# Performance work log

Hardware: AMD Instinct MI355X
Metric: run time of the kernel (lower is better)

## Reference

```python
import jax, jax.numpy as jnp
import numpy as np

N = 729        # problem variables
B = 8          # batch
K = 32         # mixing rank (hard-coded in MixingFunc)
NB = 40        # number of symmetry-basis matrices
MAX_ITER = 10  # coordinate-descent sweeps


def setup_inputs() -> dict:
    key = jax.random.key(0)
    ks = jax.random.split(key, 7)
    coeff = jax.random.normal(ks[0], (NB,), jnp.float32)
    upper = jax.random.normal(ks[1], (N,), jnp.float32)
    basis = jax.random.normal(ks[2], (NB, N, N), jnp.float32)
    z = jax.random.uniform(ks[3], (B, N), jnp.float32)
    is_input = jax.random.randint(ks[4], (B, N), 0, 2).astype(jnp.int32)
    v_init_raw = jax.random.normal(ks[5], (B, N + 1, K), jnp.float32)
    # random permutation of the N non-truth variables (indices 1..N), as in satnet init
    perm = (jax.random.permutation(ks[6], N) + 1).astype(jnp.int32)
    return dict(coeff=coeff, upper=upper, basis=basis, z=z,
                is_input=is_input, v_init_raw=v_init_raw, perm=perm)


def _build_C(coeff, upper, basis):
    # BasisFunc.forward: C = [[0, upper^T], [upper, sum_b coeff_b * basis_b]]
    center = jnp.einsum('b,bij->ij', coeff, basis)              # (N, N)
    top = jnp.concatenate([jnp.zeros((1,), upper.dtype), upper])[None, :]  # (1, N+1)
    bottom = jnp.concatenate([upper[:, None], center], axis=1)  # (N, N+1)
    return jnp.concatenate([top, bottom], axis=0)               # (N+1, N+1)


def _init_V(v_raw, z_full):
    # SATNet init: v0 = random unit truth direction; each v_i is placed on the
    # cone around v0 at angle pi*z_i using a random orthogonal direction.
    v0 = v_raw[:, 0] / jnp.linalg.norm(v_raw[:, 0], axis=-1, keepdims=True)  # (B, K)
    dot = jnp.einsum('bnk,bk->bn', v_raw, v0)
    u = v_raw - dot[..., None] * v0[:, None, :]
    u = u / jnp.maximum(jnp.linalg.norm(u, axis=-1, keepdims=True), 1e-8)
    c = jnp.cos(jnp.pi * z_full)[..., None]
    s = jnp.sin(jnp.pi * z_full)[..., None]
    V = -c * v0[:, None, :] + s * u                              # (B, N+1, K)
    V = V.at[:, 0].set(v0)                                       # truth vector pinned
    return V


def _mix(C, V, is_input_full, perm):
    # SATNet mixing coordinate descent: for each free variable i,
    #   g_i = sum_j C[j,i] v_j - C[i,i] v_i ;  v_i <- -g_i / ||g_i||
    Cdiag = jnp.diagonal(C)
    free = (is_input_full == 0)                                  # (B, N+1)

    def coord_step(V, i):
        g = jnp.einsum('j,bjk->bk', C[:, i], V) - Cdiag[i] * V[:, i]  # (B, K)
        gn = jnp.linalg.norm(g, axis=-1, keepdims=True)
        vnew = -g / jnp.maximum(gn, 1e-8)
        V = V.at[:, i].set(jnp.where(free[:, i][:, None], vnew, V[:, i]))
        return V, None

    def sweep(V, _):
        V, _ = jax.lax.scan(coord_step, V, perm)
        return V, None

    V, _ = jax.lax.scan(jax.checkpoint(sweep), V, None, length=MAX_ITER)
    return V


def reference(coeff, upper, basis, z, is_input, v_init_raw, perm):
    Bn = z.shape[0]
    C = _build_C(coeff, upper, basis)
    z_full = jnp.concatenate([jnp.ones((Bn, 1), z.dtype), z], axis=1)
    ii_full = jnp.concatenate(
        [jnp.ones((Bn, 1), is_input.dtype), is_input], axis=1)
    V = _init_V(v_init_raw, z_full)
    V = _mix(C, V, ii_full, perm)
    v0 = V[:, 0]
    cosang = jnp.clip(-jnp.einsum('bnk,bk->bn', V, v0), -1.0 + 1e-6, 1.0 - 1e-6)
    zo = jnp.arccos(cosang) / jnp.pi
    z_out = jnp.where(ii_full == 1, z_full, zo)
    return z_out[:, 1:]
```

## Files before the change

kernel.cpp:

```cpp
#include <hip/hip_runtime.h>

#define NN   729
#define NF   730
#define BV   8
#define KK   32
#define NBAS 40
#define MAXIT 10
#define PI_F 3.14159265358979323846f

#define MTH   512
#define BT    16
#define AST   448

typedef float v2f __attribute__((ext_vector_type(2)));

__device__ __forceinline__ void fma4(float4& w, float c, const float4& d) {
    w.x = fmaf(c, d.x, w.x); w.y = fmaf(c, d.y, w.y);
    w.z = fmaf(c, d.z, w.z); w.w = fmaf(c, d.w, w.w);
}

__global__ void build_C_kernel(const float* __restrict__ coeff,
                               const float* __restrict__ upper,
                               const float* __restrict__ basis,
                               float* __restrict__ Ct) {
    int idx = blockIdx.x * blockDim.x + threadIdx.x;
    if (idx >= NF * NF) return;
    int i = idx / NF, j = idx - i * NF;
    float val;
    if (i == 0) {
        val = (j == 0) ? 0.f : upper[j - 1];
    } else if (j == 0) {
        val = upper[i - 1];
    } else {
        float acc = 0.f;
        const float* bp = basis + (size_t)(i - 1) * NN + (j - 1);
        #pragma unroll 8
        for (int b = 0; b < NBAS; ++b)
            acc = fmaf(coeff[b], bp[(size_t)b * NN * NN], acc);
        val = acc;
    }
    Ct[(size_t)j * NF + i] = val;
}

__global__ void init_V_kernel(const float* __restrict__ z,
                              const float* __restrict__ vraw,
                              float* __restrict__ V) {
    int g = threadIdx.x >> 5;
    int k = threadIdx.x & 31;
    int row = blockIdx.x * 8 + g;
    int b = row / NF, n = row - b * NF;
    const float* vr = vraw + (size_t)b * NF * KK;

    float v0 = vr[k];
    float s2 = v0 * v0;
    #pragma unroll
    for (int off = 16; off; off >>= 1) s2 += __shfl_xor(s2, off, 32);
    v0 = v0 / sqrtf(s2);

    float vn = vr[(size_t)n * KK + k];
    float d = vn * v0;
    #pragma unroll
    for (int off = 16; off; off >>= 1) d += __shfl_xor(d, off, 32);
    float u = vn - d * v0;
    float un2 = u * u;
    #pragma unroll
    for (int off = 16; off; off >>= 1) un2 += __shfl_xor(un2, off, 32);
    u = u / fmaxf(sqrtf(un2), 1e-8f);

    float zf = (n == 0) ? 1.f : z[b * NN + (n - 1)];
    float c = cosf(PI_F * zf), s = sinf(PI_F * zf);
    float outv = -c * v0 + s * u;
    if (n == 0) outv = v0;
    V[((size_t)b * NF + n) * KK + k] = outv;
}

__global__ void build_act_kernel(const int* __restrict__ is_input,
                                 const int* __restrict__ perm,
                                 int* __restrict__ act, int* __restrict__ nA_arr) {
    int b = blockIdx.x, l = threadIdx.x;
    int base = 0;
    for (int c = 0; c < (NN + 63) / 64; ++c) {
        int idx = c * 64 + l;
        bool f = false; int pi = 0;
        if (idx < NN) { pi = perm[idx]; f = (is_input[b * NN + pi - 1] == 0); }
        unsigned long long m = __ballot(f);
        int pos = __popcll(m & ((1ull << l) - 1ull));
        if (f && base + pos < AST) act[b * AST + base + pos] = pi;
        base += __popcll(m);
    }
    if (base > AST) base = AST;
    if (l == 0) nA_arr[b] = base;
    for (int p = base + l; p < AST; p += 64) act[b * AST + p] = 0;
}

__global__ void gather_CactT_kernel(const float* __restrict__ Ct,
                                    const int* __restrict__ act,
                                    float* __restrict__ CactT) {
    int a = blockIdx.x, b = blockIdx.y;
    __shared__ int acts[AST];
    for (int i = threadIdx.x; i < AST; i += blockDim.x) acts[i] = act[b * AST + i];
    __syncthreads();
    const float* src = Ct + (size_t)acts[a] * NF;
    float* dst = CactT + ((size_t)b * AST + a) * AST;
    for (int t = threadIdx.x; t < AST; t += blockDim.x)
        dst[t] = src[acts[t]];
}

__global__ void init_W_kernel(const float* __restrict__ Ct,
                              const int* __restrict__ act,
                              const int* __restrict__ nA_arr,
                              const float* __restrict__ V,
                              float* __restrict__ Wc,
                              float* __restrict__ Vact) {
    int b = blockIdx.y;
    int a = blockIdx.x * 8 + (threadIdx.x >> 5);
    int k = threadIdx.x & 31;
    int nA = nA_arr[b];
    float w = 0.f;
    int ra = act[b * AST + a];
    float vv = V[((size_t)b * NF + ra) * KK + k];
    if (a < nA) {
        const float* ctr = Ct + (size_t)ra * NF;
        const float* vb = V + (size_t)b * NF * KK + k;
        float acc = 0.f;
        for (int j = 0; j < NF; ++j)
            acc = fmaf(ctr[j], vb[(size_t)j * KK], acc);
        w = acc - ctr[ra] * vv;
    }
    Wc[((size_t)b * AST + a) * KK + k] = w;
    Vact[((size_t)b * AST + a) * KK + k] = vv;
}

__device__ __forceinline__ float rowsum16(float x) {
    int y;
    y = __builtin_amdgcn_update_dpp(0, __float_as_int(x), 0x121, 0xF, 0xF, false);
    x += __int_as_float(y);
    y = __builtin_amdgcn_update_dpp(0, __float_as_int(x), 0x122, 0xF, 0xF, false);
    x += __int_as_float(y);
    y = __builtin_amdgcn_update_dpp(0, __float_as_int(x), 0x124, 0xF, 0xF, false);
    x += __int_as_float(y);
    y = __builtin_amdgcn_update_dpp(0, __float_as_int(x), 0x128, 0xF, 0xF, false);
    x += __int_as_float(y);
    return x;
}

__global__ __launch_bounds__(MTH, 2)
void mix_kernel(const float* __restrict__ CactT_g,
                const float* __restrict__ Wc_g,
                const float* __restrict__ Vact_g,
                const int* __restrict__ act_g,
                const int* __restrict__ nA_arr,
                const int* __restrict__ is_input,
                const float* __restrict__ z,
                const float* __restrict__ Vg,
                float* __restrict__ out) {
    __shared__ __align__(16) float V_c[AST * KK];
    __shared__ __align__(16) float dv_s[2][BT * KK];
    __shared__ __align__(16) float gpub[BT * KK];
    __shared__ __align__(16) float cblk_s[2][BT * BT];
    __shared__ float Cd_s[AST];
    __shared__ int   slot_s[NF];
    __shared__ float ldspad[3200];

    int b = blockIdx.x, tid = threadIdx.x;
    const float* CT = CactT_g + (size_t)b * AST * AST;
    const float* Vact = Vact_g + (size_t)b * AST * KK;
    int nA = nA_arr[b];
    int nblkp = (nA + BT - 1) / BT;
    if (nblkp < 2) nblkp = 2;
    int nAp = nblkp * BT;
    int totB = MAXIT * nblkp;

    int wid = tid >> 6;
    int l64 = tid & 63;
    int lane = tid - 64;
    int kq = lane & 7;
    int rslot = lane >> 3;
    int kp = tid & 15;

    for (int idx = tid; idx < AST * 8; idx += MTH)
        ((float4*)V_c)[idx] = ((const float4*)Vact)[idx];
    if (tid < AST) Cd_s[tid] = CT[(size_t)tid * AST + tid];
    if (tid < nA) slot_s[act_g[b * AST + tid]] = tid;
    if (tid < 256) {
        int t = tid >> 4, u = tid & 15;
        cblk_s[0][t * BT + u] = CT[(size_t)u * AST + t];
    }
    if (tid == 0) ldspad[3199] = 0.f;
    float4 w[8];
    #pragma unroll
    for (int p = 0; p < 8; ++p) {
        float4 zz = {0.f, 0.f, 0.f, 0.f};
        w[p] = zz;
        if (wid >= 1)
            w[p] = *(const float4*)&Wc_g[((size_t)b * AST + rslot + 56 * p) * KK + 4 * kq];
    }
    __syncthreads();

    for (int bi = 0; bi < totB; ++bi) {
        int blk = bi % nblkp, s0 = blk * BT;
        int pblk = (bi - 1 + nblkp) % nblkp, sp0 = pblk * BT;
        int cb = bi & 1, pv = cb ^ 1;
        int sn0 = ((bi + 1) % nblkp) * BT;

        if (wid >= 1) {
            #pragma unroll
            for (int p = 0; p < 8; ++p) {
                int a = rslot + 56 * p;
                if ((a >> 4) == blk) {
                    int u = a - s0;
                    if (bi > 0) {
                        const float* cr = CT + (size_t)a * AST + sp0;
                        float4 c0 = *(const float4*)(cr);
                        float4 c1 = *(const float4*)(cr + 4);
                        float4 c2 = *(const float4*)(cr + 8);
                        float4 c3 = *(const float4*)(cr + 12);
                        float4 d;
                        d = *(const float4*)&dv_s[pv][0  * KK + 4 * kq]; fma4(w[p], c0.x, d);
                        d = *(const float4*)&dv_s[pv][1  * KK + 4 * kq]; fma4(w[p], c0.y, d);
                        d = *(const float4*)&dv_s[pv][2  * KK + 4 * kq]; fma4(w[p], c0.z, d);
                        d = *(const float4*)&dv_s[pv][3  * KK + 4 * kq]; fma4(w[p], c0.w, d);
                        d = *(const float4*)&dv_s[pv][4  * KK + 4 * kq]; fma4(w[p], c1.x, d);
                        d = *(const float4*)&dv_s[pv][5  * KK + 4 * kq]; fma4(w[p], c1.y, d);
                        d = *(const float4*)&dv_s[pv][6  * KK + 4 * kq]; fma4(w[p], c1.z, d);
                        d = *(const float4*)&dv_s[pv][7  * KK + 4 * kq]; fma4(w[p], c1.w, d);
                        d = *(const float4*)&dv_s[pv][8  * KK + 4 * kq]; fma4(w[p], c2.x, d);
                        d = *(const float4*)&dv_s[pv][9  * KK + 4 * kq]; fma4(w[p], c2.y, d);
                        d = *(const float4*)&dv_s[pv][10 * KK + 4 * kq]; fma4(w[p], c2.z, d);
                        d = *(const float4*)&dv_s[pv][11 * KK + 4 * kq]; fma4(w[p], c2.w, d);
                        d = *(const float4*)&dv_s[pv][12 * KK + 4 * kq]; fma4(w[p], c3.x, d);
                        d = *(const float4*)&dv_s[pv][13 * KK + 4 * kq]; fma4(w[p], c3.y, d);
                        d = *(const float4*)&dv_s[pv][14 * KK + 4 * kq]; fma4(w[p], c3.z, d);
                        d = *(const float4*)&dv_s[pv][15 * KK + 4 * kq]; fma4(w[p], c3.w, d);
                    }
                    *(float4*)&gpub[u * KK + 4 * kq] = w[p];
                }
            }
        }
        __syncthreads();

        if (wid == 0) {
            float g0[BT], g1[BT], vo0[BT], vo1[BT];
            #pragma unroll
            for (int u = 0; u < BT; ++u) {
                v2f gv = *(const v2f*)&gpub[u * KK + 2 * kp];
                g0[u] = gv.x; g1[u] = gv.y;
                v2f vv = *(const v2f*)&V_c[(s0 + u) * KK + 2 * kp];
                vo0[u] = vv.x; vo1[u] = vv.y;
            }
            #pragma unroll
            for (int u = 0; u < BT; ++u) {
                int s = s0 + u;
                float n2 = fmaf(g0[u], g0[u], g1[u] * g1[u]);
                n2 = rowsum16(n2);
                float inv = -__builtin_amdgcn_rsqf(fmaxf(n2, 1e-16f));
                float msk = (s < nA) ? 1.f : 0.f;
                float d0 = fmaf(g0[u], inv, -vo0[u]) * msk;
                float d1 = fmaf(g1[u], inv, -vo1[u]) * msk;
                if (tid < 16) {
                    v2f dv2; dv2.x = d0; dv2.y = d1;
                    *(v2f*)&dv_s[cb][u * KK + 2 * kp] = dv2;
                    v2f vn2; vn2.x = vo0[u] + d0; vn2.y = vo1[u] + d1;
                    *(v2f*)&V_c[s * KK + 2 * kp] = vn2;
                }
                #pragma unroll
                for (int u2 = u + 1; u2 < BT; ++u2) {
                    float c = cblk_s[cb][u * BT + u2];
                    g0[u2] = fmaf(c, d0, g0[u2]);
                    g1[u2] = fmaf(c, d1, g1[u2]);
                }
            }
        } else {
            if (wid == 7) {
                int u = l64 & 15, q = l64 >> 4;
                float4 v = *(const float4*)&CT[(size_t)(sn0 + u) * AST + sn0 + 4 * q];
                cblk_s[pv][(4 * q + 0) * BT + u] = v.x;
                cblk_s[pv][(4 * q + 1) * BT + u] = v.y;
                cblk_s[pv][(4 * q + 2) * BT + u] = v.z;
                cblk_s[pv][(4 * q + 3) * BT + u] = v.w;
            }
            if (bi > 0) {
                #pragma unroll
                for (int h = 0; h < 2; ++h) {
                    float4 dvv[8];
                    #pragma unroll
                    for (int t = 0; t < 8; ++t)
                        dvv[t] = *(const float4*)&dv_s[pv][(8 * h + t) * KK + 4 * kq];
                    float4 cA0, cB0, cA1, cB1;
                    {
                        const float* cr = CT + (size_t)rslot * AST + sp0 + 8 * h;
                        cA0 = *(const float4*)(cr);
                        cB0 = *(const float4*)(cr + 4);
                    }
                    #pragma unroll
                    for (int p = 0; p < 8; ++p) {
                        int a = rslot + 56 * p;
                        if (p < 7) {
                            const float* cr = CT + (size_t)(a + 56) * AST + sp0 + 8 * h;
                            if (p & 1) { cA0 = *(const float4*)(cr); cB0 = *(const float4*)(cr + 4); }
                            else       { cA1 = *(const float4*)(cr); cB1 = *(const float4*)(cr + 4); }
                        }
                        float4 ca = (p & 1) ? cA1 : cA0;
                        float4 cbq = (p & 1) ? cB1 : cB0;
                        if (a < nAp && (a >> 4) != blk) {
                            fma4(w[p], ca.x,  dvv[0]);
                            fma4(w[p], ca.y,  dvv[1]);
                            fma4(w[p], ca.z,  dvv[2]);
                            fma4(w[p], ca.w,  dvv[3]);
                            fma4(w[p], cbq.x, dvv[4]);
                            fma4(w[p], cbq.y, dvv[5]);
                            fma4(w[p], cbq.z, dvv[6]);
                            fma4(w[p], cbq.w, dvv[7]);
                        }
                    }
                }
                #pragma unroll
                for (int p = 0; p < 8; ++p) {
                    int a = rslot + 56 * p;
                    if ((a >> 4) == pblk) {
                        float4 dd = *(const float4*)&dv_s[pv][(a - sp0) * KK + 4 * kq];
                        fma4(w[p], -Cd_s[a], dd);
                    }
                }
            }
        }
        __syncthreads();
    }

    int k = tid & 31, r = tid >> 5;
    float v0k = Vg[(size_t)b * NF * KK + k];
    for (int n = 1 + r; n <= NN; n += 16) {
        int ii = is_input[b * NN + n - 1];
        float res;
        if (ii == 1) {
            res = z[b * NN + n - 1];
        } else {
            int a = slot_s[n];
            float dot = V_c[a * KK + k] * v0k;
            #pragma unroll
            for (int off = 16; off; off >>= 1) dot += __shfl_xor(dot, off, 32);
            float ca = fminf(fmaxf(-dot, -1.f + 1e-6f), 1.f - 1e-6f);
            res = acosf(ca) * (1.f / PI_F);
        }
        if (k == 0) out[b * NN + n - 1] = res;
    }
}

extern "C" void kernel_launch(void* const* d_in, const int* in_sizes, int n_in,
                              void* d_out, int out_size, void* d_ws, size_t ws_size,
                              hipStream_t stream) {
    const float* coeff    = (const float*)d_in[0];
    const float* upper    = (const float*)d_in[1];
    const float* basis    = (const float*)d_in[2];
    const float* z        = (const float*)d_in[3];
    const int*   is_input = (const int*)d_in[4];
    const float* vraw     = (const float*)d_in[5];
    const int*   perm     = (const int*)d_in[6];
    float* out = (float*)d_out;

    float* ws    = (float*)d_ws;
    float* Ct    = ws;
    float* V     = Ct + (size_t)NF * NF;
    float* CactT = V + (size_t)BV * NF * KK;
    float* Wc    = CactT + (size_t)BV * AST * AST;
    float* Vact  = Wc + (size_t)BV * AST * KK;
    int*   act   = (int*)(Vact + (size_t)BV * AST * KK);
    int*   nAa   = act + BV * AST;

    build_C_kernel<<<dim3((NF * NF + 255) / 256), dim3(256), 0, stream>>>(coeff, upper, basis, Ct);
    init_V_kernel<<<dim3(730), dim3(256), 0, stream>>>(z, vraw, V);
    build_act_kernel<<<dim3(BV), dim3(64), 0, stream>>>(is_input, perm, act, nAa);
    gather_CactT_kernel<<<dim3(AST, BV), dim3(256), 0, stream>>>(Ct, act, CactT);
    init_W_kernel<<<dim3(AST / 8, BV), dim3(256), 0, stream>>>(Ct, act, nAa, V, Wc, Vact);
    mix_kernel<<<dim3(BV), dim3(MTH), 0, stream>>>(CactT, Wc, Vact, act, nAa, is_input, z, V, out);
}
```

Measured before the change: 738.8 us.

## Remove per-block publish phase by pre-publishing next block's gradients one step ahead

Drops the separate gradient-publish phase and its extra barrier in each block step. Worker waves now apply the rank-16 update to every row, including the next block, and publish that block's partial gradients into a double-buffered gpub one step early. The solver wave applies the missing previous-block correction itself, using a small transposed C tile (cminiT_s) that wave 6 prefetches. This halves the barriers per block, but the serial solver wave takes on 16x16 extra FMAs per step, and the LDS padding array is removed, which changes LDS use and occupancy.

```diff
diff --git a/kernel.cpp b/kernel.cpp
--- a/kernel.cpp
+++ b/kernel.cpp
@@ -156,11 +156,11 @@
                 float* __restrict__ out) {
     __shared__ __align__(16) float V_c[AST * KK];
     __shared__ __align__(16) float dv_s[2][BT * KK];
-    __shared__ __align__(16) float gpub[BT * KK];
+    __shared__ __align__(16) float gpub[2][BT * KK];
     __shared__ __align__(16) float cblk_s[2][BT * BT];
+    __shared__ __align__(16) float cminiT_s[2][BT * BT];
     __shared__ float Cd_s[AST];
     __shared__ int   slot_s[NF];
-    __shared__ float ldspad[3200];
 
     int b = blockIdx.x, tid = threadIdx.x;
     const float* CT = CactT_g + (size_t)b * AST * AST;
@@ -186,7 +186,6 @@
         int t = tid >> 4, u = tid & 15;
         cblk_s[0][t * BT + u] = CT[(size_t)u * AST + t];
     }
-    if (tid == 0) ldspad[3199] = 0.f;
     float4 w[8];
     #pragma unroll
     for (int p = 0; p < 8; ++p) {
@@ -195,58 +194,48 @@
         if (wid >= 1)
             w[p] = *(const float4*)&Wc_g[((size_t)b * AST + rslot + 56 * p) * KK + 4 * kq];
     }
+    if (wid >= 1) {
+        #pragma unroll
+        for (int p = 0; p < 8; ++p) {
+            int a = rslot + 56 * p;
+            if ((a >> 4) == 0)
+                *(float4*)&gpub[1][a * KK + 4 * kq] = w[p];
+        }
+    }
     __syncthreads();
 
     for (int bi = 0; bi < totB; ++bi) {
         int blk = bi % nblkp, s0 = blk * BT;
         int pblk = (bi - 1 + nblkp) % nblkp, sp0 = pblk * BT;
         int cb = bi & 1, pv = cb ^ 1;
-        int sn0 = ((bi + 1) % nblkp) * BT;
-
-        if (wid >= 1) {
-            #pragma unroll
-            for (int p = 0; p < 8; ++p) {
-                int a = rslot + 56 * p;
-                if ((a >> 4) == blk) {
-                    int u = a - s0;
-                    if (bi > 0) {
-                        const float* cr = CT + (size_t)a * AST + sp0;
-                        float4 c0 = *(const float4*)(cr);
-                        float4 c1 = *(const float4*)(cr + 4);
-                        float4 c2 = *(const float4*)(cr + 8);
-                        float4 c3 = *(const float4*)(cr + 12);
-                        float4 d;
-                        d = *(const float4*)&dv_s[pv][0  * KK + 4 * kq]; fma4(w[p], c0.x, d);
-                        d = *(const float4*)&dv_s[pv][1  * KK + 4 * kq]; fma4(w[p], c0.y, d);
-                        d = *(const float4*)&dv_s[pv][2  * KK + 4 * kq]; fma4(w[p], c0.z, d);
-                        d = *(const float4*)&dv_s[pv][3  * KK + 4 * kq]; fma4(w[p], c0.w, d);
-                        d = *(const float4*)&dv_s[pv][4  * KK + 4 * kq]; fma4(w[p], c1.x, d);
-                        d = *(const float4*)&dv_s[pv][5  * KK + 4 * kq]; fma4(w[p], c1.y, d);
-                        d = *(const float4*)&dv_s[pv][6  * KK + 4 * kq]; fma4(w[p], c1.z, d);
-                        d = *(const float4*)&dv_s[pv][7  * KK + 4 * kq]; fma4(w[p], c1.w, d);
-                        d = *(const float4*)&dv_s[pv][8  * KK + 4 * kq]; fma4(w[p], c2.x, d);
-                        d = *(const float4*)&dv_s[pv][9  * KK + 4 * kq]; fma4(w[p], c2.y, d);
-                        d = *(const float4*)&dv_s[pv][10 * KK + 4 * kq]; fma4(w[p], c2.z, d);
-                        d = *(const float4*)&dv_s[pv][11 * KK + 4 * kq]; fma4(w[p], c2.w, d);
-                        d = *(const float4*)&dv_s[pv][12 * KK + 4 * kq]; fma4(w[p], c3.x, d);
-                        d = *(const float4*)&dv_s[pv][13 * KK + 4 * kq]; fma4(w[p], c3.y, d);
-                        d = *(const float4*)&dv_s[pv][14 * KK + 4 * kq]; fma4(w[p], c3.z, d);
-                        d = *(const float4*)&dv_s[pv][15 * KK + 4 * kq]; fma4(w[p], c3.w, d);
-                    }
-                    *(float4*)&gpub[u * KK + 4 * kq] = w[p];
-                }
-            }
-        }
-        __syncthreads();
+        int nblk2 = (bi + 1) % nblkp, sn0 = nblk2 * BT;
 
         if (wid == 0) {
             float g0[BT], g1[BT], vo0[BT], vo1[BT];
             #pragma unroll
             for (int u = 0; u < BT; ++u) {
-                v2f gv = *(const v2f*)&gpub[u * KK + 2 * kp];
+                v2f gv = *(const v2f*)&gpub[pv][u * KK + 2 * kp];
                 g0[u] = gv.x; g1[u] = gv.y;
                 v2f vv = *(const v2f*)&V_c[(s0 + u) * KK + 2 * kp];
                 vo0[u] = vv.x; vo1[u] = vv.y;
+            }
+            if (bi > 0) {
+                #pragma unroll
+                for (int t = 0; t < BT; ++t) {
+                    v2f dp = *(const v2f*)&dv_s[pv][t * KK + 2 * kp];
+                    #pragma unroll
+                    for (int q = 0; q < 4; ++q) {
+                        float4 cm = *(const float4*)&cminiT_s[cb][t * BT + 4 * q];
+                        g0[4*q+0] = fmaf(cm.x, dp.x, g0[4*q+0]);
+                        g1[4*q+0] = fmaf(cm.x, dp.y, g1[4*q+0]);
+                        g0[4*q+1] = fmaf(cm.y, dp.x, g0[4*q+1]);
+                        g1[4*q+1] = fmaf(cm.y, dp.y, g1[4*q+1]);
+                        g0[4*q+2] = fmaf(cm.z, dp.x, g0[4*q+2]);
+                        g1[4*q+2] = fmaf(cm.z, dp.y, g1[4*q+2]);
+                        g0[4*q+3] = fmaf(cm.w, dp.x, g0[4*q+3]);
+                        g1[4*q+3] = fmaf(cm.w, dp.y, g1[4*q+3]);
+                    }
+                }
             }
             #pragma unroll
             for (int u = 0; u < BT; ++u) {
@@ -271,6 +260,14 @@
                 }
             }
         } else {
+            if (wid == 6) {
+                int u = l64 & 15, q = l64 >> 4;
+                float4 v = *(const float4*)&CT[(size_t)(sn0 + u) * AST + s0 + 4 * q];
+                cminiT_s[pv][(4 * q + 0) * BT + u] = v.x;
+                cminiT_s[pv][(4 * q + 1) * BT + u] = v.y;
+                cminiT_s[pv][(4 * q + 2) * BT + u] = v.z;
+                cminiT_s[pv][(4 * q + 3) * BT + u] = v.w;
+            }
             if (wid == 7) {
                 int u = l64 & 15, q = l64 >> 4;
                 float4 v = *(const float4*)&CT[(size_t)(sn0 + u) * AST + sn0 + 4 * q];
@@ -302,7 +299,7 @@
                         }
                         float4 ca = (p & 1) ? cA1 : cA0;
                         float4 cbq = (p & 1) ? cB1 : cB0;
-                        if (a < nAp && (a >> 4) != blk) {
+                        if (a < nAp) {
                             fma4(w[p], ca.x,  dvv[0]);
                             fma4(w[p], ca.y,  dvv[1]);
                             fma4(w[p], ca.z,  dvv[2]);
@@ -322,6 +319,12 @@
                         fma4(w[p], -Cd_s[a], dd);
                     }
                 }
+            }
+            #pragma unroll
+            for (int p = 0; p < 8; ++p) {
+                int a = rslot + 56 * p;
+                if ((a >> 4) == nblk2)
+                    *(float4*)&gpub[cb][(a - sn0) * KK + 4 * kq] = w[p];
             }
         }
         __syncthreads();
```

Measured after the change: 858.1 us. 16.2% more time.
